# Kernel tuning notes

Hardware: AMD Instinct MI355X
Metric: run time of the kernel (lower is better)

The kernel has to match this reference:

```python
import jax, jax.numpy as jnp
import numpy as np

P, N, K, F = 4, 4096, 2, 256
E = 8            # num_experts
H = 4 * 256      # ffn_ratio * output_dim
OUT = 256        # output_dim


def setup_inputs() -> dict:
    key = jax.random.key(0)
    ks = jax.random.split(key, 9)
    s = 0.02
    return {
        "x_parts": jax.random.normal(ks[0], (P, N, K, F), dtype=jnp.float32),
        "selected_experts": jax.random.randint(ks[1], (P, N, K), 0, E, dtype=jnp.int64),
        # SwiGLU: gate and up projections F -> H (per expert)
        "Wg": jax.random.normal(ks[2], (E, F, H), dtype=jnp.float32) * s,
        "bg": jnp.zeros((E, H), dtype=jnp.float32),
        "Wu": jax.random.normal(ks[3], (E, F, H), dtype=jnp.float32) * s,
        "bu": jnp.zeros((E, H), dtype=jnp.float32),
        # man_fc (Euclidean): Linear(H,H) -> ReLU -> Linear(H,OUT)
        "W1": jax.random.normal(ks[4], (E, H, H), dtype=jnp.float32) * s,
        "b1": jnp.zeros((E, H), dtype=jnp.float32),
        "W2": jax.random.normal(ks[5], (E, H, OUT), dtype=jnp.float32) * s,
        "b2": jnp.zeros((E, OUT), dtype=jnp.float32),
    }


def _expert(x, Wg, bg, Wu, bu, W1, b1, W2, b2):
    # x: [T, F] -> [T, OUT]; SwiGLU then Linear-ReLU-Linear (Euclidean man_fc)
    h = jax.nn.silu(x @ Wg + bg) * (x @ Wu + bu)   # [T, H]
    h = jax.nn.relu(h @ W1 + b1)                    # [T, H]
    return h @ W2 + b2                              # [T, OUT]


def reference(x_parts, selected_experts, Wg, bg, Wu, bu, W1, b1, W2, b2):
    # Each (p, i, k) token-copy is processed by expert selected_experts[p,i,k];
    # dense masked combine replaces the Python-level gather/scatter loops.
    x = x_parts.reshape(-1, F)                      # [T, F], T = P*N*K
    sel = selected_experts.reshape(-1)              # [T]
    out = jnp.zeros((x.shape[0], OUT), dtype=x_parts.dtype)
    for e in range(E):
        y = _expert(x, Wg[e], bg[e], Wu[e], bu[e], W1[e], b1[e], W2[e], b2[e])
        out = out + jnp.where((sel == e)[:, None], y, 0.0)
    return out.reshape(P, N, K, OUT)
```

## Files before the change

### kernel.cpp

```cpp
#include <hip/hip_runtime.h>
#include <hip/hip_bf16.h>
#include <cstdint>
#include <cstddef>

#define NTOK 32768
#define FD   256
#define HD   1024
#define OD   256
#define NEXP 8

#define BM 128
#define BN 128
#define BK 64
#define MAXRT 34
#define RT8 34

typedef __bf16 bf16;
typedef __bf16 bf16x8 __attribute__((ext_vector_type(8)));
typedef __bf16 bf16x4 __attribute__((ext_vector_type(4)));
typedef float  f32x4  __attribute__((ext_vector_type(4)));

__device__ __forceinline__ void cp16(const void* g, void* l) {
    __builtin_amdgcn_global_load_lds(
        (const __attribute__((address_space(1))) void*)g,
        (__attribute__((address_space(3))) void*)l, 16, 0, 0);
}

static const size_t O_CNT  = 0;
static const size_t O_CUR  = 64;
static const size_t O_OFF  = 128;
static const size_t O_NT   = 192;
static const size_t O_TE   = 1024;
static const size_t O_TR   = 3072;
static const size_t O_PERM = 5120;
static const size_t O_XP   = 136192;
static const size_t O_WG   = 16913408;
static const size_t O_WU   = 21107712;
static const size_t O_W1   = 25302016;
static const size_t O_W2   = 42079232;
static const size_t O_H    = 46273536;
static const size_t O_H2   = 113382400;

__global__ void k_hist(const int* __restrict__ sel, int* __restrict__ cnt) {
    __shared__ int lcnt[NEXP];
    if (threadIdx.x < NEXP) lcnt[threadIdx.x] = 0;
    __syncthreads();
    int t = blockIdx.x * 256 + threadIdx.x;
    atomicAdd(&lcnt[sel[t]], 1);
    __syncthreads();
    if (threadIdx.x < NEXP) atomicAdd(&cnt[threadIdx.x], lcnt[threadIdx.x]);
}

__global__ void k_plan(const int* __restrict__ cnt, int* __restrict__ off,
                       int* __restrict__ tileE, int* __restrict__ tileR,
                       int* __restrict__ nt) {
    if (threadIdx.x == 0 && blockIdx.x == 0) {
        int o = 0;
        for (int e = 0; e < NEXP; e++) { off[e] = o; o += cnt[e]; }
        off[NEXP] = o;
        int n = 0;
        for (int e = 0; e < NEXP; e++) {
            int c = cnt[e];
            int nte = (c + BM - 1) / BM;
            for (int r = 0; r < nte; r++) { tileE[n] = e; tileR[n] = r; n++; }
        }
        *nt = n;
    }
}

__global__ void k_scatter(const int* __restrict__ sel, const int* __restrict__ off,
                          int* __restrict__ cur, int* __restrict__ perm) {
    __shared__ int lcnt[NEXP];
    __shared__ int lbase[NEXP];
    if (threadIdx.x < NEXP) lcnt[threadIdx.x] = 0;
    __syncthreads();
    int t = blockIdx.x * 256 + threadIdx.x;
    int e = sel[t];
    int rank = atomicAdd(&lcnt[e], 1);
    __syncthreads();
    if (threadIdx.x < NEXP)
        lbase[threadIdx.x] = atomicAdd(&cur[threadIdx.x], lcnt[threadIdx.x]);
    __syncthreads();
    perm[off[e] + lbase[e] + rank] = t;
}

__global__ void k_gather(const float* __restrict__ x, const int* __restrict__ perm,
                         bf16* __restrict__ Xp) {
    int gid = blockIdx.x * 256 + threadIdx.x;
    int pos = gid >> 6;
    int c   = gid & 63;
    int tok = perm[pos];
    float4 v = ((const float4*)x)[(size_t)tok * 64 + c];
    bf16x4 o;
    o.x = (bf16)v.x; o.y = (bf16)v.y; o.z = (bf16)v.z; o.w = (bf16)v.w;
    *(bf16x4*)&Xp[(size_t)pos * FD + c * 4] = o;
}

#define TPE 448
__global__ void k_transpose_all(const float* __restrict__ Wg, bf16* __restrict__ Wgt,
                                const float* __restrict__ Wu, bf16* __restrict__ Wut,
                                const float* __restrict__ W1, bf16* __restrict__ W1t,
                                const float* __restrict__ W2, bf16* __restrict__ W2t) {
    __shared__ float tile[64][65];
    int b  = blockIdx.x;
    int e  = b / TPE;
    int tt = b % TPE;
    const float* Ws; bf16* Wd; int K, N;
    if (tt < 64)       { Ws = Wg; Wd = Wgt; K = FD; N = HD; }
    else if (tt < 128) { Ws = Wu; Wd = Wut; K = FD; N = HD; tt -= 64; }
    else if (tt < 384) { Ws = W1; Wd = W1t; K = HD; N = HD; tt -= 128; }
    else               { Ws = W2; Wd = W2t; K = HD; N = OD; tt -= 384; }
    int nk = K / 64;
    int k0 = (tt % nk) * 64, n0 = (tt / nk) * 64;
    Ws += (size_t)e * K * N;
    Wd += (size_t)e * K * N;
    int t = threadIdx.x;
    for (int q = 0; q < 4; q++) {
        int lin = t + q * 256;
        int r = lin >> 4, c4 = (lin & 15) * 4;
        float4 v = *(const float4*)&Ws[(size_t)(k0 + r) * N + n0 + c4];
        tile[r][c4] = v.x; tile[r][c4+1] = v.y; tile[r][c4+2] = v.z; tile[r][c4+3] = v.w;
    }
    __syncthreads();
    for (int q = 0; q < 2; q++) {
        int lin = t + q * 256;
        int n = lin >> 3, k8 = (lin & 7) * 8;
        bf16x8 o;
        for (int i = 0; i < 8; i++) o[i] = (bf16)tile[k8 + i][n];
        *(bf16x8*)&Wd[(size_t)(n0 + n) * K + k0 + k8] = o;
    }
}


#define DECODE_TILE(NTY, BNE)                                                  \
    int L = blockIdx.x;                                                        \
    int xcd = L & 7; int tq = L >> 3;                                          \
    int ny  = tq % (NTY); int Rhi = tq / (NTY);                                \
    int R   = Rhi * 8 + xcd;                                                   \
    if (R >= *ntp) return;                                                     \
    int e    = tileE[R];                                                       \
    int row0 = tileR[R] * BM;                                                  \
    int base = off[e];                                                         \
    int valid = off[e + 1] - base - row0; if (valid > BM) valid = BM;          \
    int n0 = ny * (BNE);                                                       \
    int tid = threadIdx.x;                                                     \
    int lane = tid & 63, wv = tid >> 6;                                        \
    int wm = wv & 1, wn = wv >> 1;                                             \
    int lr = lane & 15, qd = lane >> 4;

#define GEMM_KLOOP(KDIM)                                                       \
    for (int k0 = 0; k0 < (KDIM); k0 += BK) {                                  \
        for (int s = 0; s < 4; s++) {                                          \
            int ci = tid + s * 256;                                            \
            int row = ci >> 3;                                                 \
            int jg  = (ci & 7) ^ (row & 7);                                    \
            int mc  = row < valid ? row : valid - 1;                           \
            cp16(Ab + (size_t)mc  * (KDIM) + k0 + jg * 8, &As[ci * 8]);        \
            cp16(Bb + (size_t)row * (KDIM) + k0 + jg * 8, &Bs[ci * 8]);        \
        }                                                                      \
        __syncthreads();                                                       \
        for (int ks = 0; ks < 2; ks++) {                                       \
            bf16x8 af[4], bfr[4];                                              \
            for (int i = 0; i < 4; i++) {                                      \
                int row = wm * 64 + i * 16 + lr;                               \
                int sl  = (ks * 4 + qd) ^ (row & 7);                           \
                af[i] = *(const bf16x8*)&As[row * BK + sl * 8];                \
            }                                                                  \
            for (int j = 0; j < 4; j++) {                                      \
                int row = wn * 64 + j * 16 + lr;                               \
                int sl  = (ks * 4 + qd) ^ (row & 7);                           \
                bfr[j] = *(const bf16x8*)&Bs[row * BK + sl * 8];               \
            }                                                                  \
            for (int i = 0; i < 4; i++)                                        \
                for (int j = 0; j < 4; j++)                                    \
                    acc[i][j] = __builtin_amdgcn_mfma_f32_16x16x32_bf16(       \
                        af[i], bfr[j], acc[i][j], 0, 0, 0);                    \
        }                                                                      \
        __syncthreads();                                                       \
    }

__global__ __launch_bounds__(256, 3) void k_swiglu(
    const bf16* __restrict__ Xp, const bf16* __restrict__ Wgt, const bf16* __restrict__ Wut,
    const float* __restrict__ bg, const float* __restrict__ bu, bf16* __restrict__ Hbuf,
    const int* __restrict__ tileE, const int* __restrict__ tileR,
    const int* __restrict__ off, const int* __restrict__ ntp)
{
    __shared__ bf16 As [BM * BK];
    __shared__ bf16 Bgs[64 * BK];
    __shared__ bf16 Bus[64 * BK];
    DECODE_TILE(16, 64)

    f32x4 accg[4][2] = {};
    f32x4 accu[4][2] = {};
    const bf16* Ab  = Xp  + (size_t)(base + row0) * FD;
    const bf16* Bgb = Wgt + ((size_t)e * HD + n0) * FD;
    const bf16* Bub = Wut + ((size_t)e * HD + n0) * FD;

    for (int k0 = 0; k0 < FD; k0 += BK) {
        for (int s = 0; s < 4; s++) {
            int ci = tid + s * 256;
            int row = ci >> 3;
            int jg  = (ci & 7) ^ (row & 7);
            int mc  = row < valid ? row : valid - 1;
            cp16(Ab + (size_t)mc * FD + k0 + jg * 8, &As[ci * 8]);
        }
        for (int s = 0; s < 2; s++) {
            int ci = tid + s * 256;
            int row = ci >> 3;
            int jg  = (ci & 7) ^ (row & 7);
            cp16(Bgb + (size_t)row * FD + k0 + jg * 8, &Bgs[ci * 8]);
            cp16(Bub + (size_t)row * FD + k0 + jg * 8, &Bus[ci * 8]);
        }
        __syncthreads();
        for (int ks = 0; ks < 2; ks++) {
            bf16x8 af[4], bgf[2], buf[2];
            for (int i = 0; i < 4; i++) {
                int row = wm * 64 + i * 16 + lr;
                int sl  = (ks * 4 + qd) ^ (row & 7);
                af[i] = *(const bf16x8*)&As[row * BK + sl * 8];
            }
            for (int j = 0; j < 2; j++) {
                int row = wn * 32 + j * 16 + lr;
                int sl  = (ks * 4 + qd) ^ (row & 7);
                bgf[j] = *(const bf16x8*)&Bgs[row * BK + sl * 8];
                buf[j] = *(const bf16x8*)&Bus[row * BK + sl * 8];
            }
            for (int i = 0; i < 4; i++)
                for (int j = 0; j < 2; j++) {
                    accg[i][j] = __builtin_amdgcn_mfma_f32_16x16x32_bf16(af[i], bgf[j], accg[i][j], 0, 0, 0);
                    accu[i][j] = __builtin_amdgcn_mfma_f32_16x16x32_bf16(af[i], buf[j], accu[i][j], 0, 0, 0);
                }
        }
        __syncthreads();
    }
    for (int i = 0; i < 4; i++) {
        int rb = wm * 64 + i * 16 + qd * 4;
        for (int r = 0; r < 4; r++) {
            int m = rb + r;
            if (m >= valid) continue;
            size_t orow = (size_t)(base + row0 + m) * HD;
            for (int j = 0; j < 2; j++) {
                int n = n0 + wn * 32 + j * 16 + lr;
                float g = accg[i][j][r] + bg[e * HD + n];
                float u = accu[i][j][r] + bu[e * HD + n];
                float h = g * u / (1.f + __expf(-g));
                Hbuf[orow + n] = (bf16)h;
            }
        }
    }
}

__global__ __launch_bounds__(256, 3) void k_gemm2(
    const bf16* __restrict__ Ain, const bf16* __restrict__ Bt, const float* __restrict__ bias,
    bf16* __restrict__ Out,
    const int* __restrict__ tileE, const int* __restrict__ tileR,
    const int* __restrict__ off, const int* __restrict__ ntp)
{
    __shared__ bf16 As[BM * BK];
    __shared__ bf16 Bs[BN * BK];
    DECODE_TILE(8, BN)
    f32x4 acc[4][4] = {};
    const bf16* Ab = Ain + (size_t)(base + row0) * HD;
    const bf16* Bb = Bt  + ((size_t)e * HD + n0) * HD;
    GEMM_KLOOP(HD)
    for (int i = 0; i < 4; i++) {
        int rb = wm * 64 + i * 16 + qd * 4;
        for (int r = 0; r < 4; r++) {
            int m = rb + r;
            if (m >= valid) continue;
            size_t orow = (size_t)(base + row0 + m) * HD;
            for (int j = 0; j < 4; j++) {
                int n = n0 + wn * 64 + j * 16 + lr;
                float v = acc[i][j][r] + bias[e * HD + n];
                Out[orow + n] = (bf16)(v > 0.f ? v : 0.f);
            }
        }
    }
}

__global__ __launch_bounds__(256, 3) void k_gemm3(
    const bf16* __restrict__ Ain, const bf16* __restrict__ Bt, const float* __restrict__ bias,
    float* __restrict__ out, const int* __restrict__ perm,
    const int* __restrict__ tileE, const int* __restrict__ tileR,
    const int* __restrict__ off, const int* __restrict__ ntp)
{
    __shared__ bf16 As[BM * BK];
    __shared__ bf16 Bs[BN * BK];
    DECODE_TILE(2, BN)
    f32x4 acc[4][4] = {};
    const bf16* Ab = Ain + (size_t)(base + row0) * HD;
    const bf16* Bb = Bt  + ((size_t)e * OD + n0) * HD;
    GEMM_KLOOP(HD)
    for (int i = 0; i < 4; i++) {
        int rb = wm * 64 + i * 16 + qd * 4;
        for (int r = 0; r < 4; r++) {
            int m = rb + r;
            if (m >= valid) continue;
            int tok = perm[base + row0 + m];
            size_t orow = (size_t)tok * OD;
            for (int j = 0; j < 4; j++) {
                int n = n0 + wn * 64 + j * 16 + lr;
                out[orow + n] = acc[i][j][r] + bias[e * OD + n];
            }
        }
    }
}

extern "C" void kernel_launch(void* const* d_in, const int* in_sizes, int n_in,
                              void* d_out, int out_size, void* d_ws, size_t ws_size,
                              hipStream_t stream) {
    const float* x   = (const float*)d_in[0];
    const int*   sel = (const int*)d_in[1];
    const float* Wg  = (const float*)d_in[2];
    const float* bg  = (const float*)d_in[3];
    const float* Wu  = (const float*)d_in[4];
    const float* bu  = (const float*)d_in[5];
    const float* W1  = (const float*)d_in[6];
    const float* b1  = (const float*)d_in[7];
    const float* W2  = (const float*)d_in[8];
    const float* b2  = (const float*)d_in[9];
    float* out = (float*)d_out;

    char* ws = (char*)d_ws;
    int* cnt   = (int*)(ws + O_CNT);
    int* cur   = (int*)(ws + O_CUR);
    int* off   = (int*)(ws + O_OFF);
    int* nt    = (int*)(ws + O_NT);
    int* tileE = (int*)(ws + O_TE);
    int* tileR = (int*)(ws + O_TR);
    int* perm  = (int*)(ws + O_PERM);
    bf16* Xp   = (bf16*)(ws + O_XP);
    bf16* Wgt  = (bf16*)(ws + O_WG);
    bf16* Wut  = (bf16*)(ws + O_WU);
    bf16* W1t  = (bf16*)(ws + O_W1);
    bf16* W2t  = (bf16*)(ws + O_W2);
    bf16* Hbuf = (bf16*)(ws + O_H);
    bf16* H2   = (bf16*)(ws + O_H2);

    hipMemsetAsync(ws, 0, 256, stream);

    k_hist   <<<NTOK / 256, 256, 0, stream>>>(sel, cnt);
    k_plan   <<<1, 64, 0, stream>>>(cnt, off, tileE, tileR, nt);
    k_scatter<<<NTOK / 256, 256, 0, stream>>>(sel, off, cur, perm);
    k_gather <<<NTOK * 64 / 256, 256, 0, stream>>>(x, perm, Xp);

    k_transpose_all<<<NEXP * TPE, 256, 0, stream>>>(Wg, Wgt, Wu, Wut, W1, W1t, W2, W2t);

    k_swiglu<<<RT8 * 16 * 8, 256, 0, stream>>>(Xp, Wgt, Wut, bg, bu, Hbuf,
                                               tileE, tileR, off, nt);
    k_gemm2 <<<RT8 * 8 * 8, 256, 0, stream>>>(Hbuf, W1t, b1, H2,
                                              tileE, tileR, off, nt);
    k_gemm3 <<<RT8 * 2 * 8, 256, 0, stream>>>(H2, W2t, b2, out, perm,
                                              tileE, tileR, off, nt);
}
```

Before: 334.3 us.

## Replace gemm2 with 256x256-tile 512-thread kernel using phased LDS double-buffering

The H×H ReLU GEMM moves to a new kernel with 256-row by 256-column tiles, 8 waves and 128KB of dynamic LDS. Global-to-LDS loads are double-buffered and interleaved with four MFMA phases per K step, using explicit waitcnt, barriers and setprio, and the LDS layout is XOR-swizzled. A second tile plan with 256-row tiles is added, and tiles are mapped to XCDs. This aims to raise data reuse and overlap memory with compute, at the cost of fewer, larger blocks (one per CU) and more padding waste on partial expert tiles.

```diff
diff --git a/kernel.cpp b/kernel.cpp
--- a/kernel.cpp
+++ b/kernel.cpp
@@ -12,8 +12,8 @@
 #define BM 128
 #define BN 128
 #define BK 64
-#define MAXRT 34
 #define RT8 34
+#define RT2_8 17
 
 typedef __bf16 bf16;
 typedef __bf16 bf16x8 __attribute__((ext_vector_type(8)));
@@ -30,8 +30,11 @@
 static const size_t O_CUR  = 64;
 static const size_t O_OFF  = 128;
 static const size_t O_NT   = 192;
+static const size_t O_NT2  = 196;
 static const size_t O_TE   = 1024;
+static const size_t O_TE2  = 2112;
 static const size_t O_TR   = 3072;
+static const size_t O_TR2  = 4160;
 static const size_t O_PERM = 5120;
 static const size_t O_XP   = 136192;
 static const size_t O_WG   = 16913408;
@@ -53,7 +56,9 @@
 
 __global__ void k_plan(const int* __restrict__ cnt, int* __restrict__ off,
                        int* __restrict__ tileE, int* __restrict__ tileR,
-                       int* __restrict__ nt) {
+                       int* __restrict__ nt,
+                       int* __restrict__ tileE2, int* __restrict__ tileR2,
+                       int* __restrict__ nt2) {
     if (threadIdx.x == 0 && blockIdx.x == 0) {
         int o = 0;
         for (int e = 0; e < NEXP; e++) { off[e] = o; o += cnt[e]; }
@@ -65,6 +70,13 @@
             for (int r = 0; r < nte; r++) { tileE[n] = e; tileR[n] = r; n++; }
         }
         *nt = n;
+        int n2 = 0;
+        for (int e = 0; e < NEXP; e++) {
+            int c = cnt[e];
+            int nte = (c + 255) / 256;
+            for (int r = 0; r < nte; r++) { tileE2[n2] = e; tileR2[n2] = r; n2++; }
+        }
+        *nt2 = n2;
     }
 }
 
@@ -250,28 +262,122 @@
     }
 }
 
-__global__ __launch_bounds__(256, 3) void k_gemm2(
-    const bf16* __restrict__ Ain, const bf16* __restrict__ Bt, const float* __restrict__ bias,
-    bf16* __restrict__ Out,
-    const int* __restrict__ tileE, const int* __restrict__ tileR,
-    const int* __restrict__ off, const int* __restrict__ ntp)
+
+#define STG_A(buf, h, k0)                                                      \
+    { _Pragma("unroll") for (int s = 0; s < 2; s++) {                          \
+        int rr = (h) * 128 + s * 64 + rbase;                                   \
+        int mr = rr < valid ? rr : valid - 1;                                  \
+        cp16(Ab + (size_t)mr * HD + (k0) + jg8,                                \
+             &sm[(buf) * 16384 + (h) * 8192 + (s * 512 + tid) * 8]); } }
+
+#define STG_B(buf, h, k0)                                                      \
+    { _Pragma("unroll") for (int s = 0; s < 2; s++) {                          \
+        int rr = (h) * 128 + s * 64 + rbase;                                   \
+        cp16(Bb + (size_t)rr * HD + (k0) + jg8,                                \
+             &sm[32768 + (buf) * 16384 + (h) * 8192 + (s * 512 + tid) * 8]); } }
+
+#define PHASE(p, STAGE, DOVW)                                                  \
+    {                                                                          \
+        bf16x8 af[2][2];                                                       \
+        _Pragma("unroll") for (int ii = 0; ii < 2; ii++) {                     \
+            int ro = b * 16384 + aB + (2 * (p) + ii) * 1024;                   \
+            af[ii][0] = *(const bf16x8*)&sm[ro + sl0];                         \
+            af[ii][1] = *(const bf16x8*)&sm[ro + sl1];                         \
+        }                                                                      \
+        STAGE;                                                                 \
+        if (DOVW) { asm volatile("s_waitcnt vmcnt(4)" ::: "memory"); }         \
+        asm volatile("" ::: "memory");                                         \
+        __builtin_amdgcn_s_barrier();                                          \
+        asm volatile("s_waitcnt lgkmcnt(0)" ::: "memory");                     \
+        __builtin_amdgcn_sched_barrier(0);                                     \
+        __builtin_amdgcn_s_setprio(1);                                         \
+        _Pragma("unroll") for (int ii = 0; ii < 2; ii++)                       \
+        _Pragma("unroll") for (int j = 0; j < 4; j++) {                        \
+            acc[2 * (p) + ii][j] = __builtin_amdgcn_mfma_f32_16x16x32_bf16(    \
+                af[ii][0], bfr[j][0], acc[2 * (p) + ii][j], 0, 0, 0);          \
+            acc[2 * (p) + ii][j] = __builtin_amdgcn_mfma_f32_16x16x32_bf16(    \
+                af[ii][1], bfr[j][1], acc[2 * (p) + ii][j], 0, 0, 0);          \
+        }                                                                      \
+        __builtin_amdgcn_s_setprio(0);                                         \
+        asm volatile("" ::: "memory");                                         \
+        __builtin_amdgcn_s_barrier();                                          \
+        asm volatile("" ::: "memory");                                         \
+    }
+
+__global__ __launch_bounds__(512, 1) void k_gemm2_8ph(
+    const bf16* __restrict__ Ain, const bf16* __restrict__ Bt,
+    const float* __restrict__ bias, bf16* __restrict__ Out,
+    const int* __restrict__ tileE2, const int* __restrict__ tileR2,
+    const int* __restrict__ off, const int* __restrict__ ntp2)
 {
-    __shared__ bf16 As[BM * BK];
-    __shared__ bf16 Bs[BN * BK];
-    DECODE_TILE(8, BN)
-    f32x4 acc[4][4] = {};
+    extern __shared__ bf16 sm[];
+    int L = blockIdx.x;
+    int xcd = L & 7, tq = L >> 3;
+    int ny = tq & 3, Rhi = tq >> 2;
+    int R = Rhi * 8 + xcd;
+    if (R >= *ntp2) return;
+    int e    = tileE2[R];
+    int row0 = tileR2[R] * 256;
+    int base = off[e];
+    int valid = off[e + 1] - base - row0; if (valid > 256) valid = 256;
+    int n0 = ny * 256;
+    int tid = threadIdx.x;
+    int lane = tid & 63, wv = tid >> 6;
+    int wm = wv >> 2, wn = wv & 3;
+    int lr = lane & 15, qd = lane >> 4;
+    int sl0 = (qd ^ (lr & 7)) * 8;
+    int sl1 = ((4 + qd) ^ (lr & 7)) * 8;
+    int aB = (wm * 128 + lr) * 64;
+    int bB = (wn * 64 + lr) * 64;
+    int rbase = tid >> 3;
+    int jg8 = ((tid & 7) ^ (rbase & 7)) * 8;
+
     const bf16* Ab = Ain + (size_t)(base + row0) * HD;
-    const bf16* Bb = Bt  + ((size_t)e * HD + n0) * HD;
-    GEMM_KLOOP(HD)
-    for (int i = 0; i < 4; i++) {
-        int rb = wm * 64 + i * 16 + qd * 4;
+    const bf16* Bb = Bt + ((size_t)e * HD + n0) * HD;
+
+    f32x4 acc[8][4] = {};
+
+    STG_B(0, 0, 0) STG_B(0, 1, 0)
+    STG_A(0, 0, 0) STG_A(0, 1, 0)
+    STG_B(1, 0, 64) STG_B(1, 1, 64)
+    asm volatile("s_waitcnt vmcnt(4)" ::: "memory");
+    asm volatile("" ::: "memory");
+    __builtin_amdgcn_s_barrier();
+    asm volatile("" ::: "memory");
+
+    for (int t = 0; t < 16; t++) {
+        int b = t & 1;
+        int kA = (t + 1 < 16) ? (t + 1) * 64 : 0;
+        int kB = (t + 2 < 16) ? (t + 2) * 64 : 0;
+        bf16x8 bfr[4][2];
+        #pragma unroll
+        for (int j = 0; j < 4; j++) {
+            int ro = 32768 + b * 16384 + bB + j * 1024;
+            bfr[j][0] = *(const bf16x8*)&sm[ro + sl0];
+            bfr[j][1] = *(const bf16x8*)&sm[ro + sl1];
+        }
+        PHASE(0, STG_A(b ^ 1, 0, kA), 0)
+        PHASE(1, STG_A(b ^ 1, 1, kA), 0)
+        PHASE(2, STG_B(b, 0, kB), 0)
+        PHASE(3, STG_B(b, 1, kB), 1)
+    }
+    asm volatile("s_waitcnt vmcnt(0)" ::: "memory");
+
+    float bj[4];
+    #pragma unroll
+    for (int j = 0; j < 4; j++) bj[j] = bias[e * HD + n0 + wn * 64 + j * 16 + lr];
+    #pragma unroll
+    for (int i = 0; i < 8; i++) {
+        int rb = wm * 128 + i * 16 + qd * 4;
+        #pragma unroll
         for (int r = 0; r < 4; r++) {
             int m = rb + r;
             if (m >= valid) continue;
             size_t orow = (size_t)(base + row0 + m) * HD;
+            #pragma unroll
             for (int j = 0; j < 4; j++) {
                 int n = n0 + wn * 64 + j * 16 + lr;
-                float v = acc[i][j][r] + bias[e * HD + n];
+                float v = acc[i][j][r] + bj[j];
                 Out[orow + n] = (bf16)(v > 0.f ? v : 0.f);
             }
         }
@@ -322,25 +428,35 @@
     float* out = (float*)d_out;
 
     char* ws = (char*)d_ws;
-    int* cnt   = (int*)(ws + O_CNT);
-    int* cur   = (int*)(ws + O_CUR);
-    int* off   = (int*)(ws + O_OFF);
-    int* nt    = (int*)(ws + O_NT);
-    int* tileE = (int*)(ws + O_TE);
-    int* tileR = (int*)(ws + O_TR);
-    int* perm  = (int*)(ws + O_PERM);
-    bf16* Xp   = (bf16*)(ws + O_XP);
-    bf16* Wgt  = (bf16*)(ws + O_WG);
-    bf16* Wut  = (bf16*)(ws + O_WU);
-    bf16* W1t  = (bf16*)(ws + O_W1);
-    bf16* W2t  = (bf16*)(ws + O_W2);
-    bf16* Hbuf = (bf16*)(ws + O_H);
-    bf16* H2   = (bf16*)(ws + O_H2);
+    int* cnt    = (int*)(ws + O_CNT);
+    int* cur    = (int*)(ws + O_CUR);
+    int* off    = (int*)(ws + O_OFF);
+    int* nt     = (int*)(ws + O_NT);
+    int* nt2    = (int*)(ws + O_NT2);
+    int* tileE  = (int*)(ws + O_TE);
+    int* tileE2 = (int*)(ws + O_TE2);
+    int* tileR  = (int*)(ws + O_TR);
+    int* tileR2 = (int*)(ws + O_TR2);
+    int* perm   = (int*)(ws + O_PERM);
+    bf16* Xp    = (bf16*)(ws + O_XP);
+    bf16* Wgt   = (bf16*)(ws + O_WG);
+    bf16* Wut   = (bf16*)(ws + O_WU);
+    bf16* W1t   = (bf16*)(ws + O_W1);
+    bf16* W2t   = (bf16*)(ws + O_W2);
+    bf16* Hbuf  = (bf16*)(ws + O_H);
+    bf16* H2    = (bf16*)(ws + O_H2);
+
+    static bool s_attr = false;
+    if (!s_attr) {
+        hipFuncSetAttribute((const void*)k_gemm2_8ph,
+                            hipFuncAttributeMaxDynamicSharedMemorySize, 131072);
+        s_attr = true;
+    }
 
     hipMemsetAsync(ws, 0, 256, stream);
 
     k_hist   <<<NTOK / 256, 256, 0, stream>>>(sel, cnt);
-    k_plan   <<<1, 64, 0, stream>>>(cnt, off, tileE, tileR, nt);
+    k_plan   <<<1, 64, 0, stream>>>(cnt, off, tileE, tileR, nt, tileE2, tileR2, nt2);
     k_scatter<<<NTOK / 256, 256, 0, stream>>>(sel, off, cur, perm);
     k_gather <<<NTOK * 64 / 256, 256, 0, stream>>>(x, perm, Xp);
 
@@ -348,8 +464,8 @@
 
     k_swiglu<<<RT8 * 16 * 8, 256, 0, stream>>>(Xp, Wgt, Wut, bg, bu, Hbuf,
                                                tileE, tileR, off, nt);
-    k_gemm2 <<<RT8 * 8 * 8, 256, 0, stream>>>(Hbuf, W1t, b1, H2,
-                                              tileE, tileR, off, nt);
+    k_gemm2_8ph<<<RT2_8 * 4 * 8, 512, 131072, stream>>>(Hbuf, W1t, b1, H2,
+                                                        tileE2, tileR2, off, nt2);
     k_gemm3 <<<RT8 * 2 * 8, 256, 0, stream>>>(H2, W2t, b2, out, perm,
                                               tileE, tileR, off, nt);
 }
```

Result: no change. 339.3 us (+1.5%).
